# Performance work log

Measured on AMD Instinct MI355X. Metric: run time of the kernel, lower is better.

Reference implementation:

```python
import jax, jax.numpy as jnp
import numpy as np

B, C, H, W = 4, 64, 64, 64
C8 = C // 8
OC = 64
K9 = 9


def setup_inputs() -> dict:
    key = jax.random.key(0)
    ks = jax.random.split(key, 8)
    x = jax.random.normal(ks[0], (B, C, H, W), dtype=jnp.float32)
    qw = jax.random.normal(ks[1], (C8, C), dtype=jnp.float32) * 0.05   # 1x1 conv weight
    qb = jax.random.normal(ks[2], (C8,), dtype=jnp.float32) * 0.05
    kw = jax.random.normal(ks[3], (C8, C), dtype=jnp.float32) * 0.05
    kb = jax.random.normal(ks[4], (C8,), dtype=jnp.float32) * 0.05
    gamma = jax.random.normal(ks[5], (1,), dtype=jnp.float32) * 0.1
    weight = jax.random.normal(ks[6], (OC, C, K9), dtype=jnp.float32) * 0.05
    bias = jnp.full((OC,), 0.1, dtype=jnp.float32)
    return {"x": x, "qw": qw, "qb": qb, "kw": kw, "kb": kb,
            "gamma": gamma, "weight": weight, "bias": bias}


def reference(x, qw, qb, kw, kb, gamma, weight, bias):
    b, c, h, w = x.shape
    hw = h * w
    # 1x1 convs -> (B, C8, HW)
    xf = x.reshape(b, c, hw)
    q = jnp.einsum('dc,bcn->bdn', qw, xf) + qb[None, :, None]
    k = jnp.einsum('dc,bcn->bdn', kw, xf) + kb[None, :, None]
    # energy[b,t,s] = <key[:,t], query[:,s]>  -> (B, HW, HW)
    energy = jnp.einsum('bdt,bds->bts', k, q)
    # top-9 source positions per target t; the torch boolean-mask gather
    # selects them in ascending index order, so sort the indices.
    _, idx = jax.lax.top_k(energy, K9)          # (B, HW, 9)
    idx = jnp.sort(idx, axis=-1)
    # gather x at selected positions: (B, HW, 9, C)
    x_t = xf.transpose(0, 2, 1)                 # (B, HW, C)
    gathered = jnp.take_along_axis(x_t[:, None, :, :], idx[:, :, :, None], axis=2)
    # out[b,o,j] = sum_{c,k} gathered[b,j,k,c] * weight[o,c,k] + bias[o]
    out = jnp.einsum('bjkc,ock->boj', gathered, weight) + bias[None, :, None]
    out = jax.nn.relu(out).reshape(b, c, h, w)
    return gamma[0] * out + x
```

## Files before the change

### kernel.cpp

```cpp
#include <hip/hip_runtime.h>
#include <math.h>

#define HW 4096
#define NB 4
#define LCAP 64

typedef unsigned short ushort_t;
typedef unsigned int uint_t;
typedef __attribute__((ext_vector_type(8))) _Float16 f16x8;
typedef __attribute__((ext_vector_type(4))) float f32x4;

__device__ __forceinline__ ushort_t f2h(float f) {
  _Float16 h = (_Float16)f;
  return *(ushort_t*)&h;
}

__device__ __forceinline__ float dot8(float4 klo, float4 khi, const float* qp) {
  float4 q0 = *(const float4*)qp;
  float4 q1 = *(const float4*)(qp + 4);
  float e = klo.x * q0.x;
  e = fmaf(klo.y, q0.y, e);
  e = fmaf(klo.z, q0.z, e);
  e = fmaf(klo.w, q0.w, e);
  e = fmaf(khi.x, q1.x, e);
  e = fmaf(khi.y, q1.y, e);
  e = fmaf(khi.z, q1.z, e);
  e = fmaf(khi.w, q1.w, e);
  return e;
}
__device__ __forceinline__ float dot8v(float4 klo, float4 khi, float4 q0, float4 q1) {
  float e = klo.x * q0.x;
  e = fmaf(klo.y, q0.y, e);
  e = fmaf(klo.z, q0.z, e);
  e = fmaf(klo.w, q0.w, e);
  e = fmaf(khi.x, q1.x, e);
  e = fmaf(khi.y, q1.y, e);
  e = fmaf(khi.z, q1.z, e);
  e = fmaf(khi.w, q1.w, e);
  return e;
}

__global__ __launch_bounds__(256) void qk_kernel(
    const float* __restrict__ x, const float* __restrict__ qw,
    const float* __restrict__ qb, const float* __restrict__ kw,
    const float* __restrict__ kb, const float* __restrict__ w,
    float* __restrict__ q_t, float* __restrict__ k_t,
    ushort_t* __restrict__ xT, ushort_t* __restrict__ wt_h) {
  __shared__ float red[4][64][17];
  __shared__ float sqwT[512], skwT[512];
  int b = blockIdx.y;
  int sl = threadIdx.x & 63;
  int cg = threadIdx.x >> 6;
  int s = blockIdx.x * 64 + sl;

  {
    int bid = blockIdx.y * 64 + blockIdx.x;
    int gid = bid * 256 + threadIdx.x;
    if (gid < 64 * 64 * 9) {
      int o = gid / 576, rem = gid % 576, c = rem / 9, k = rem % 9;
      wt_h[(k * 64 + o) * 64 + c] = f2h(w[gid]);
    }
  }

  for (int i = threadIdx.x; i < 512; i += 256) {
    int c = i >> 3, d = i & 7;
    sqwT[i] = qw[d * 64 + c];
    skwT[i] = kw[d * 64 + c];
  }
  __syncthreads();

  float qa[8], ka[8];
  ushort_t h16[16];
#pragma unroll
  for (int d = 0; d < 8; ++d) { qa[d] = 0.f; ka[d] = 0.f; }
  const float* xp = x + ((size_t)b * 64 + cg * 16) * HW + s;
#pragma unroll
  for (int c = 0; c < 16; ++c) {
    float xv = xp[(size_t)c * HW];
    h16[c] = f2h(xv);
    int cc = cg * 16 + c;
    const float4 qw0 = *(const float4*)&sqwT[cc * 8];
    const float4 qw1 = *(const float4*)&sqwT[cc * 8 + 4];
    const float4 kw0 = *(const float4*)&skwT[cc * 8];
    const float4 kw1 = *(const float4*)&skwT[cc * 8 + 4];
    qa[0] = fmaf(qw0.x, xv, qa[0]); qa[1] = fmaf(qw0.y, xv, qa[1]);
    qa[2] = fmaf(qw0.z, xv, qa[2]); qa[3] = fmaf(qw0.w, xv, qa[3]);
    qa[4] = fmaf(qw1.x, xv, qa[4]); qa[5] = fmaf(qw1.y, xv, qa[5]);
    qa[6] = fmaf(qw1.z, xv, qa[6]); qa[7] = fmaf(qw1.w, xv, qa[7]);
    ka[0] = fmaf(kw0.x, xv, ka[0]); ka[1] = fmaf(kw0.y, xv, ka[1]);
    ka[2] = fmaf(kw0.z, xv, ka[2]); ka[3] = fmaf(kw0.w, xv, ka[3]);
    ka[4] = fmaf(kw1.x, xv, ka[4]); ka[5] = fmaf(kw1.y, xv, ka[5]);
    ka[6] = fmaf(kw1.z, xv, ka[6]); ka[7] = fmaf(kw1.w, xv, ka[7]);
  }
  {
    ushort_t* xo = xT + (((size_t)b * HW + s) * 64 + cg * 16);
    *(uint4*)&xo[0] = *(const uint4*)&h16[0];
    *(uint4*)&xo[8] = *(const uint4*)&h16[8];
  }
#pragma unroll
  for (int d = 0; d < 8; ++d) {
    red[cg][sl][d] = qa[d];
    red[cg][sl][8 + d] = ka[d];
  }
  __syncthreads();

#pragma unroll
  for (int r = 0; r < 4; ++r) {
    int f = r * 256 + threadIdx.x;
    int slf = f >> 4, dd = f & 15;
    float sum = red[0][slf][dd] + red[1][slf][dd] + red[2][slf][dd] + red[3][slf][dd];
    int ss_ = blockIdx.x * 64 + slf;
    if (dd < 8)
      q_t[((size_t)b * HW + ss_) * 8 + dd] = sum + qb[dd];
    else
      k_t[((size_t)b * HW + ss_) * 8 + (dd - 8)] = sum + kb[dd - 8];
  }
}

__global__ __launch_bounds__(256) void mid_kernel(
    const float* __restrict__ q_t, const float* __restrict__ k_t,
    float* __restrict__ maxima) {
  __shared__ float qs[512];
  int blk = blockIdx.x;
  int tid = threadIdx.x;
  int b = blk >> 8;
  int rem = blk & 255;
  int ch = rem >> 2;
  int tg = rem & 3;
  int lane = tid & 63;
  int w = tid >> 6;
  int t0 = tg * 1024 + w * 256 + 4 * lane;

  const float* kp = k_t + ((size_t)b * HW + t0) * 8;
  float4 ka0 = *(const float4*)(kp);      float4 ka1 = *(const float4*)(kp + 4);
  float4 kb0 = *(const float4*)(kp + 8);  float4 kb1 = *(const float4*)(kp + 12);
  float4 kc0 = *(const float4*)(kp + 16); float4 kc1 = *(const float4*)(kp + 20);
  float4 kd0 = *(const float4*)(kp + 24); float4 kd1 = *(const float4*)(kp + 28);

  if (tid < 128)
    *(float4*)&qs[tid * 4] =
        *(const float4*)&q_t[((size_t)b * HW + ch * 64) * 8 + tid * 4];
  __syncthreads();

  float m0 = -INFINITY, m1 = -INFINITY, m2 = -INFINITY, m3 = -INFINITY;
#pragma unroll 4
  for (int i = 0; i < 64; ++i) {
    float4 q0 = *(const float4*)&qs[i * 8];
    float4 q1 = *(const float4*)&qs[i * 8 + 4];
    m0 = fmaxf(m0, dot8v(ka0, ka1, q0, q1));
    m1 = fmaxf(m1, dot8v(kb0, kb1, q0, q1));
    m2 = fmaxf(m2, dot8v(kc0, kc1, q0, q1));
    m3 = fmaxf(m3, dot8v(kd0, kd1, q0, q1));
  }
  *(float4*)&maxima[((size_t)b * 64 + ch) * HW + t0] =
      make_float4(m0, m1, m2, m3);
}

__global__ __launch_bounds__(256) void topk_gather_kernel(
    const float* __restrict__ q_t, const float* __restrict__ k_t,
    const float* __restrict__ maxima, const ushort_t* __restrict__ xT,
    const ushort_t* __restrict__ wt_h, const float* __restrict__ bias,
    const float* __restrict__ gamma, const float* __restrict__ x,
    float* __restrict__ out) {
  __shared__ float ldsM[64 * 17];
  __shared__ int sArr[4][LCAP];
  __shared__ float eArr[4][LCAP];
  __shared__ int sIdx[16][9];
  __shared__ float T[64 * 17];
  __shared__ __align__(16) ushort_t Gf[16 * 648];
  int b = blockIdx.y;
  int lane = threadIdx.x & 63;
  int w = threadIdx.x >> 6;
  int t0 = blockIdx.x * 16;

#pragma unroll
  for (int it = 0; it < 4; ++it) {
    int idx = it * 256 + threadIdx.x;
    int ch = idx >> 4, dt = idx & 15;
    ldsM[ch * 17 + dt] = maxima[((size_t)b * 64 + ch) * HW + t0 + dt];
  }
  __syncthreads();

  float val[4], keepm[4], tau_[4];
#pragma unroll
  for (int ti = 0; ti < 4; ++ti) {
    val[ti] = ldsM[lane * 17 + (w * 4 + ti)];
    keepm[ti] = val[ti];
  }
#pragma unroll
  for (int r = 0; r < 9; ++r) {
    float wmax[4];
#pragma unroll
    for (int ti = 0; ti < 4; ++ti) wmax[ti] = val[ti];
#pragma unroll
    for (int off = 1; off < 64; off <<= 1) {
#pragma unroll
      for (int ti = 0; ti < 4; ++ti)
        wmax[ti] = fmaxf(wmax[ti], __shfl_xor(wmax[ti], off, 64));
    }
#pragma unroll
    for (int ti = 0; ti < 4; ++ti) {
      tau_[ti] = wmax[ti];
      unsigned long long m = __ballot(val[ti] == wmax[ti]);
      if (lane == (int)__builtin_ctzll(m)) val[ti] = -INFINITY;
    }
  }

#pragma unroll 1
  for (int ti = 0; ti < 4; ++ti) {
    int jl = w * 4 + ti;
    int t = t0 + jl;

    const float* kp = k_t + ((size_t)b * HW + t) * 8;
    float4 klo = *(const float4*)kp;
    float4 khi = *(const float4*)(kp + 4);
    float tauv = tau_[ti];

    unsigned long long mask = __ballot(keepm[ti] >= tauv);
    int cnt = 0;
#pragma unroll 1
    while (mask) {
      int nbp = (int)__popcll(mask);
      int nb = nbp < 9 ? nbp : 9;
      int id0 = (int)__builtin_ctzll(mask);
      int ids[9];
      unsigned long long m2 = mask;
#pragma unroll
      for (int i = 0; i < 9; ++i) {
        ids[i] = m2 ? (int)__builtin_ctzll(m2) : id0;
        m2 &= (m2 - 1);
      }
      mask = m2;
      float ev[9];
#pragma unroll
      for (int i = 0; i < 9; ++i)
        ev[i] = dot8(klo, khi,
                     q_t + ((size_t)b * HW + ids[i] * 64 + lane) * 8);
#pragma unroll
      for (int i = 0; i < 9; ++i) {
        if (i < nb) {
          bool keep = ev[i] >= tauv;
          unsigned long long km = __ballot(keep);
          if (keep) {
            int pos = cnt + (int)__popcll(km & ((1ull << lane) - 1ull));
            if (pos < LCAP) {
              sArr[w][pos] = ids[i] * 64 + lane;
              eArr[w][pos] = ev[i];
            }
          }
          cnt += (int)__popcll(km);
        }
      }
    }
    if (cnt > LCAP) cnt = LCAP;

    float em = -INFINITY; int sm = 0x7fffffff;
    if (lane < cnt) { em = eArr[w][lane]; sm = sArr[w][lane]; }
    int rank = 0;
    for (int i = 0; i < cnt; ++i) {
      float ei = eArr[w][i];
      int si = sArr[w][i];
      rank += ((ei > em) || (ei == em && si < sm)) ? 1 : 0;
    }
    bool sel = (lane < cnt) && (rank < 9);
    unsigned long long smask = __ballot(sel);
    int pos = (int)__popcll(smask & ((1ull << lane) - 1ull));
    if (sel) sIdx[jl][pos] = sm;
  }
  __syncthreads();

  {
    const ushort_t* xTb = xT + (size_t)b * HW * 64;
#pragma unroll
    for (int i = 0; i < 9; ++i) {
      int pr = i * 256 + threadIdx.x;
      int pair = pr >> 4;
      int sub = pr & 15;
      int t = pair / 9, k = pair - t * 9;
      int p = sIdx[t][k];
      *(uint2*)&Gf[t * 648 + k * 72 + sub * 4] =
          *(const uint2*)&xTb[(size_t)p * 64 + sub * 4];
    }
  }
  __syncthreads();

  {
    int lr = lane & 15, lg = lane >> 4;
    f32x4 acc = {0.f, 0.f, 0.f, 0.f};
    const ushort_t* wbase = wt_h + ((size_t)(w * 16 + lr)) * 64 + lg * 8;
#pragma unroll
    for (int k = 0; k < 9; ++k) {
      f16x8 a0 = *(const f16x8*)&Gf[lr * 648 + k * 72 + lg * 8];
      f16x8 a1 = *(const f16x8*)&Gf[lr * 648 + k * 72 + 32 + lg * 8];
      f16x8 b0 = *(const f16x8*)&wbase[(size_t)k * 4096];
      f16x8 b1 = *(const f16x8*)&wbase[(size_t)k * 4096 + 32];
      acc = __builtin_amdgcn_mfma_f32_16x16x32_f16(a0, b0, acc, 0, 0, 0);
      acc = __builtin_amdgcn_mfma_f32_16x16x32_f16(a1, b1, acc, 0, 0, 0);
    }
    float g = gamma[0];
    float bo = bias[w * 16 + lr];
#pragma unroll
    for (int r = 0; r < 4; ++r)
      T[(w * 16 + lr) * 17 + lg * 4 + r] = g * fmaxf(acc[r] + bo, 0.f);
  }
  __syncthreads();

  for (int f = threadIdx.x; f < 1024; f += 256) {
    int o = f >> 4, jl = f & 15;
    size_t gi = ((size_t)b * 64 + o) * HW + t0 + jl;
    out[gi] = T[o * 17 + jl] + x[gi];
  }
}

extern "C" void kernel_launch(void* const* d_in, const int* in_sizes, int n_in,
                              void* d_out, int out_size, void* d_ws, size_t ws_size,
                              hipStream_t stream) {
  const float* x = (const float*)d_in[0];
  const float* qw = (const float*)d_in[1];
  const float* qb = (const float*)d_in[2];
  const float* kw = (const float*)d_in[3];
  const float* kb = (const float*)d_in[4];
  const float* gamma = (const float*)d_in[5];
  const float* weight = (const float*)d_in[6];
  const float* bias = (const float*)d_in[7];
  float* out = (float*)d_out;

  char* ws = (char*)d_ws;
  float* q_t = (float*)(ws);
  float* k_t = (float*)(ws + 524288);
  float* maxima = (float*)(ws + 1048576);
  ushort_t* xT = (ushort_t*)(ws + 5242880);
  ushort_t* wt_h = (ushort_t*)(ws + 7340032);

  hipLaunchKernelGGL(qk_kernel, dim3(64, 4), dim3(256), 0, stream,
                     x, qw, qb, kw, kb, weight, q_t, k_t, xT, wt_h);
  hipLaunchKernelGGL(mid_kernel, dim3(1024), dim3(256), 0, stream,
                     q_t, k_t, maxima);
  hipLaunchKernelGGL(topk_gather_kernel, dim3(256, 4), dim3(256), 0, stream,
                     q_t, k_t, maxima, xT, wt_h, bias, gamma, x, out);
}
```

Measured before the change: 124.1 us.

## Process one target per wave in topk kernel with rank-based threshold

Restructures the top-k gather kernel so each block handles 4 targets with one target per wave, instead of 16 targets with 4 per wave. The grid grows fourfold, and the per-target serial loop goes away. The 9-round shuffle-max threshold selection is replaced by a rank count over LDS followed by a single min-reduction. Launch bounds add an occupancy hint and LDS use shrinks. The trade-off is that the MFMA now computes 16 rows but only 4 are useful, wasting three quarters of the tensor work, and weight reads are repeated across more blocks.

```diff
diff --git a/kernel.cpp b/kernel.cpp
--- a/kernel.cpp
+++ b/kernel.cpp
@@ -156,104 +156,83 @@
       make_float4(m0, m1, m2, m3);
 }
 
-__global__ __launch_bounds__(256) void topk_gather_kernel(
+__global__ __launch_bounds__(256, 8) void topk_gather_kernel(
     const float* __restrict__ q_t, const float* __restrict__ k_t,
     const float* __restrict__ maxima, const ushort_t* __restrict__ xT,
     const ushort_t* __restrict__ wt_h, const float* __restrict__ bias,
     const float* __restrict__ gamma, const float* __restrict__ x,
     float* __restrict__ out) {
-  __shared__ float ldsM[64 * 17];
+  __shared__ float ldsM[64 * 5];
   __shared__ int sArr[4][LCAP];
   __shared__ float eArr[4][LCAP];
-  __shared__ int sIdx[16][9];
-  __shared__ float T[64 * 17];
-  __shared__ __align__(16) ushort_t Gf[16 * 648];
+  __shared__ int sIdx[4][9];
+  __shared__ float T[64 * 5];
+  __shared__ __align__(16) ushort_t Gf[4 * 648];
   int b = blockIdx.y;
   int lane = threadIdx.x & 63;
   int w = threadIdx.x >> 6;
-  int t0 = blockIdx.x * 16;
-
-#pragma unroll
-  for (int it = 0; it < 4; ++it) {
-    int idx = it * 256 + threadIdx.x;
-    int ch = idx >> 4, dt = idx & 15;
-    ldsM[ch * 17 + dt] = maxima[((size_t)b * 64 + ch) * HW + t0 + dt];
-  }
-  __syncthreads();
-
-  float val[4], keepm[4], tau_[4];
-#pragma unroll
-  for (int ti = 0; ti < 4; ++ti) {
-    val[ti] = ldsM[lane * 17 + (w * 4 + ti)];
-    keepm[ti] = val[ti];
-  }
-#pragma unroll
-  for (int r = 0; r < 9; ++r) {
-    float wmax[4];
-#pragma unroll
-    for (int ti = 0; ti < 4; ++ti) wmax[ti] = val[ti];
-#pragma unroll
-    for (int off = 1; off < 64; off <<= 1) {
-#pragma unroll
-      for (int ti = 0; ti < 4; ++ti)
-        wmax[ti] = fmaxf(wmax[ti], __shfl_xor(wmax[ti], off, 64));
-    }
-#pragma unroll
-    for (int ti = 0; ti < 4; ++ti) {
-      tau_[ti] = wmax[ti];
-      unsigned long long m = __ballot(val[ti] == wmax[ti]);
-      if (lane == (int)__builtin_ctzll(m)) val[ti] = -INFINITY;
-    }
-  }
-
+  int t0 = blockIdx.x * 4;
+  int t = t0 + w;
+
+  {
+    int ch = threadIdx.x >> 2, dt = threadIdx.x & 3;
+    ldsM[ch * 5 + dt] = maxima[((size_t)b * 64 + ch) * HW + t0 + dt];
+  }
+  __syncthreads();
+
+  float val = ldsM[lane * 5 + w];
+  int rnk = 0;
+#pragma unroll
+  for (int ch = 0; ch < 64; ++ch)
+    rnk += (ldsM[ch * 5 + w] > val) ? 1 : 0;
+  float tv = (rnk < 9) ? val : INFINITY;
+#pragma unroll
+  for (int off = 1; off < 64; off <<= 1)
+    tv = fminf(tv, __shfl_xor(tv, off, 64));
+  float tauv = tv;
+
+  const float* kp = k_t + ((size_t)b * HW + t) * 8;
+  float4 klo = *(const float4*)kp;
+  float4 khi = *(const float4*)(kp + 4);
+
+  unsigned long long mask = __ballot(val >= tauv);
+  int cnt = 0;
 #pragma unroll 1
-  for (int ti = 0; ti < 4; ++ti) {
-    int jl = w * 4 + ti;
-    int t = t0 + jl;
-
-    const float* kp = k_t + ((size_t)b * HW + t) * 8;
-    float4 klo = *(const float4*)kp;
-    float4 khi = *(const float4*)(kp + 4);
-    float tauv = tau_[ti];
-
-    unsigned long long mask = __ballot(keepm[ti] >= tauv);
-    int cnt = 0;
-#pragma unroll 1
-    while (mask) {
-      int nbp = (int)__popcll(mask);
-      int nb = nbp < 9 ? nbp : 9;
-      int id0 = (int)__builtin_ctzll(mask);
-      int ids[9];
-      unsigned long long m2 = mask;
-#pragma unroll
-      for (int i = 0; i < 9; ++i) {
-        ids[i] = m2 ? (int)__builtin_ctzll(m2) : id0;
-        m2 &= (m2 - 1);
+  while (mask) {
+    int nbp = (int)__popcll(mask);
+    int nb = nbp < 9 ? nbp : 9;
+    int id0 = (int)__builtin_ctzll(mask);
+    int ids[9];
+    unsigned long long m2 = mask;
+#pragma unroll
+    for (int i = 0; i < 9; ++i) {
+      ids[i] = m2 ? (int)__builtin_ctzll(m2) : id0;
+      m2 &= (m2 - 1);
+    }
+    mask = m2;
+    float ev[9];
+#pragma unroll
+    for (int i = 0; i < 9; ++i)
+      ev[i] = dot8(klo, khi, q_t + ((size_t)b * HW + ids[i] * 64 + lane) * 8);
+#pragma unroll
+    for (int i = 0; i < 9; ++i) {
+      if (i < nb) {
+        bool keep = ev[i] >= tauv;
+        unsigned long long km = __ballot(keep);
+        if (keep) {
+          int pos = cnt + (int)__popcll(km & ((1ull << lane) - 1ull));
+          if (pos < LCAP) {
+            sArr[w][pos] = ids[i] * 64 + lane;
+            eArr[w][pos] = ev[i];
+          }
+        }
+        cnt += (int)__popcll(km);
       }
-      mask = m2;
-      float ev[9];
-#pragma unroll
-      for (int i = 0; i < 9; ++i)
-        ev[i] = dot8(klo, khi,
-                     q_t + ((size_t)b * HW + ids[i] * 64 + lane) * 8);
-#pragma unroll
-      for (int i = 0; i < 9; ++i) {
-        if (i < nb) {
-          bool keep = ev[i] >= tauv;
-          unsigned long long km = __ballot(keep);
-          if (keep) {
-            int pos = cnt + (int)__popcll(km & ((1ull << lane) - 1ull));
-            if (pos < LCAP) {
-              sArr[w][pos] = ids[i] * 64 + lane;
-              eArr[w][pos] = ev[i];
-            }
-          }
-          cnt += (int)__popcll(km);
-        }
-      }
-    }
-    if (cnt > LCAP) cnt = LCAP;
-
+    }
+  }
+  if (cnt > LCAP) cnt = LCAP;
+
+  {
     float em = -INFINITY; int sm = 0x7fffffff;
     if (lane < cnt) { em = eArr[w][lane]; sm = sArr[w][lane]; }
     int rank = 0;
@@ -265,21 +244,21 @@
     bool sel = (lane < cnt) && (rank < 9);
     unsigned long long smask = __ballot(sel);
     int pos = (int)__popcll(smask & ((1ull << lane) - 1ull));
-    if (sel) sIdx[jl][pos] = sm;
+    if (sel) sIdx[w][pos] = sm;
   }
   __syncthreads();
 
   {
     const ushort_t* xTb = xT + (size_t)b * HW * 64;
 #pragma unroll
-    for (int i = 0; i < 9; ++i) {
-      int pr = i * 256 + threadIdx.x;
-      int pair = pr >> 4;
-      int sub = pr & 15;
-      int t = pair / 9, k = pair - t * 9;
-      int p = sIdx[t][k];
-      *(uint2*)&Gf[t * 648 + k * 72 + sub * 4] =
-          *(const uint2*)&xTb[(size_t)p * 64 + sub * 4];
+    for (int i = 0; i < 3; ++i) {
+      int idx = i * 64 + lane;
+      if (idx < 144) {
+        int k = idx >> 4, sub = idx & 15;
+        int p = sIdx[w][k];
+        *(uint2*)&Gf[w * 648 + k * 72 + sub * 4] =
+            *(const uint2*)&xTb[(size_t)p * 64 + sub * 4];
+      }
     }
   }
   __syncthreads();
@@ -290,25 +269,27 @@
     const ushort_t* wbase = wt_h + ((size_t)(w * 16 + lr)) * 64 + lg * 8;
 #pragma unroll
     for (int k = 0; k < 9; ++k) {
-      f16x8 a0 = *(const f16x8*)&Gf[lr * 648 + k * 72 + lg * 8];
-      f16x8 a1 = *(const f16x8*)&Gf[lr * 648 + k * 72 + 32 + lg * 8];
+      f16x8 a0 = *(const f16x8*)&Gf[(lr & 3) * 648 + k * 72 + lg * 8];
+      f16x8 a1 = *(const f16x8*)&Gf[(lr & 3) * 648 + k * 72 + 32 + lg * 8];
       f16x8 b0 = *(const f16x8*)&wbase[(size_t)k * 4096];
       f16x8 b1 = *(const f16x8*)&wbase[(size_t)k * 4096 + 32];
       acc = __builtin_amdgcn_mfma_f32_16x16x32_f16(a0, b0, acc, 0, 0, 0);
       acc = __builtin_amdgcn_mfma_f32_16x16x32_f16(a1, b1, acc, 0, 0, 0);
     }
-    float g = gamma[0];
-    float bo = bias[w * 16 + lr];
-#pragma unroll
-    for (int r = 0; r < 4; ++r)
-      T[(w * 16 + lr) * 17 + lg * 4 + r] = g * fmaxf(acc[r] + bo, 0.f);
-  }
-  __syncthreads();
-
-  for (int f = threadIdx.x; f < 1024; f += 256) {
-    int o = f >> 4, jl = f & 15;
+    if (lg == 0) {
+      float g = gamma[0];
+      float bo = bias[w * 16 + lr];
+#pragma unroll
+      for (int r = 0; r < 4; ++r)
+        T[(w * 16 + lr) * 5 + r] = g * fmaxf(acc[r] + bo, 0.f);
+    }
+  }
+  __syncthreads();
+
+  {
+    int o = threadIdx.x >> 2, jl = threadIdx.x & 3;
     size_t gi = ((size_t)b * 64 + o) * HW + t0 + jl;
-    out[gi] = T[o * 17 + jl] + x[gi];
+    out[gi] = T[o * 5 + jl] + x[gi];
   }
 }
 
@@ -336,6 +317,6 @@
                      x, qw, qb, kw, kb, weight, q_t, k_t, xT, wt_h);
   hipLaunchKernelGGL(mid_kernel, dim3(1024), dim3(256), 0, stream,
                      q_t, k_t, maxima);
-  hipLaunchKernelGGL(topk_gather_kernel, dim3(256, 4), dim3(256), 0, stream,
+  hipLaunchKernelGGL(topk_gather_kernel, dim3(1024, 4), dim3(256), 0, stream,
                      q_t, k_t, maxima, xT, wt_h, bias, gamma, x, out);
 }
```

Measured after the change: 179.6 us. 1.45x slower.
